# Kernel tuning notes

Measured on AMD Instinct MI355X. Metric: run time of the kernel, lower is better.

The kernel has to match this reference:

```python
import jax, jax.numpy as jnp
import numpy as np

N = 12288
IN_C = 64
OUT_C = 64
NEG_INF = -1.0e9

def setup_inputs() -> dict:
    key = jax.random.key(0)
    k1, k2, k3, k4 = jax.random.split(key, 4)
    x = jax.random.normal(k1, (N, IN_C), dtype=jnp.float32)
    edge_index = jax.random.randint(k2, (N, N), 0, 2, dtype=jnp.int32)
    # xavier-ish scaling for params
    weight_w = jax.random.normal(k3, (IN_C, OUT_C), dtype=jnp.float32) * (1.0 / np.sqrt(IN_C))
    weight_a = jax.random.normal(k4, (2 * OUT_C, 1), dtype=jnp.float32) * (1.0 / np.sqrt(OUT_C))
    bias = jnp.zeros((OUT_C,), dtype=jnp.float32)
    return {"x": x, "edge_index": edge_index, "weight_w": weight_w,
            "weight_a": weight_a, "bias": bias}

def reference(x, edge_index, weight_w, weight_a, bias):
    wh = x @ weight_w                              # [N, out]
    a_src = weight_a[:OUT_C, 0]                    # [out]
    a_dst = weight_a[OUT_C:, 0]                    # [out]
    # rank-1 additive score: e[i,j] = <wh_i, a_src> + <wh_j, a_dst>
    e = (wh @ a_src)[:, None] + (wh @ a_dst)[None, :]   # [N, N]
    e = jax.nn.leaky_relu(e, negative_slope=0.01)        # torch LeakyReLU default
    scores = jnp.where(edge_index > 0, e, NEG_INF)
    attention = jax.nn.softmax(scores, axis=1)           # row-wise
    out = attention @ wh                                  # [N, out]
    return out + bias
```

## Files before the change

kernel.cpp:

```cpp
#include <hip/hip_runtime.h>
#include <hip/hip_bf16.h>
#include <cstddef>
#include <cstdint>

#define Nn 12288
#define MSTRIDE 260
#define DSTOFF (2 * 16 * MSTRIDE)
#define LOG2E 1.44269504088896340736f

typedef __bf16 bf16x8 __attribute__((ext_vector_type(8)));
typedef float  f32x4  __attribute__((ext_vector_type(4)));
typedef int    i32x4  __attribute__((ext_vector_type(4)));

__device__ __forceinline__ void gload_lds16(const void* g, void* l) {
    __builtin_amdgcn_global_load_lds(
        (const __attribute__((address_space(1))) void*)g,
        (__attribute__((address_space(3))) void*)l, 16, 0, 0 );
}
__device__ __forceinline__ void gload_lds4(const void* g, void* l) {
    __builtin_amdgcn_global_load_lds(
        (const __attribute__((address_space(1))) void*)g,
        (__attribute__((address_space(3))) void*)l, 4, 0, 0);
}

__global__ __launch_bounds__(256) void prep_kernel(
    const float* __restrict__ x, const float* __restrict__ W,
    const float* __restrict__ wa, __bf16* __restrict__ whB,
    float* __restrict__ src, float* __restrict__ dst)
{
    __shared__ float  Wl[64 * 64];
    __shared__ float  Xl[64 * 64];
    __shared__ __bf16 whl[64 * 72];
    int t = threadIdx.x;
    int R0 = blockIdx.x * 64;
    for (int i = t; i < 4096; i += 256) {
        Wl[i] = W[i];
        Xl[i] = x[(size_t)R0 * 64 + i];
    }
    __syncthreads();
    int c   = t & 63;
    int r16 = (t >> 6) * 16;
    float vals[16];
    #pragma unroll
    for (int k = 0; k < 16; ++k) vals[k] = 0.f;
    #pragma unroll 16
    for (int kk = 0; kk < 64; ++kk) {
        float wv = Wl[kk * 64 + c];
        #pragma unroll
        for (int k = 0; k < 16; ++k)
            vals[k] = fmaf(Xl[(r16 + k) * 64 + kk], wv, vals[k]);
    }
    #pragma unroll
    for (int k = 0; k < 16; ++k) whl[c * 72 + r16 + k] = (__bf16)vals[k];
    __syncthreads();
    if (t < 64) {
        float s = 0.f, d = 0.f;
        #pragma unroll 16
        for (int cc = 0; cc < 64; ++cc) {
            float v = (float)whl[cc * 72 + t];
            s = fmaf(v, wa[cc], s);
            d = fmaf(v, wa[64 + cc], d);
        }
        src[R0 + t] = s * LOG2E;
        dst[R0 + t] = d * LOG2E;
    }
    #pragma unroll
    for (int gg = 0; gg < 2; ++gg) {
        int gidx   = t * 2 + gg;
        int jc_loc = gidx >> 8;
        int q      = (gidx >> 6) & 3;
        int lane   = gidx & 63;
        int crow   = (lane & 15) + 16 * q;
        int jrow   = jc_loc * 32 + (lane >> 4) * 8;
        bf16x8 v = *(const bf16x8*)&whl[crow * 72 + jrow];
        int jc = blockIdx.x * 2 + jc_loc;
        *(bf16x8*)&whB[((size_t)(jc * 4 + q) * 64 + lane) * 8] = v;
    }
}

__global__ __launch_bounds__(256) void attn_kernel(
    const int* __restrict__ mask, const __bf16* __restrict__ whB,
    const float* __restrict__ src, const float* __restrict__ dstv,
    const float* __restrict__ bias, float* __restrict__ out)
{
    __shared__ int lm[DSTOFF + 2 * 256];

    int t    = threadIdx.x;
    int lane = t & 63;
    int wid  = t >> 6;
    int g    = blockIdx.x;
    int row  = lane & 15;
    int kg   = lane >> 4;
    int jl   = kg * 8;

    float srow = src[g * 16 + row];
    asm volatile("" :: "v"(srow));

    bf16x8 vones;
    #pragma unroll
    for (int e = 0; e < 8; ++e) vones[e] = (__bf16)1.0f;

    i32x4 bset[2][8];
    f32x4 acc0 = {0.f, 0.f, 0.f, 0.f}, acc1 = acc0, acc2 = acc0, acc3 = acc0;
    f32x4 accZ = acc0;

#define STAGE(B, TT)                                                          \
    do {                                                                      \
        _Pragma("unroll")                                                     \
        for (int rr = 0; rr < 4; ++rr) {                                      \
            int rs = wid * 4 + rr;                                            \
            gload_lds16(mask + (size_t)(g * 16 + rs) * Nn + (TT) * 256 +      \
                            lane * 4,                                         \
                        &lm[(B) * 4160 + rs * MSTRIDE]);                      \
        }                                                                     \
        gload_lds4(dstv + (TT) * 256 + wid * 64 + lane,                       \
                   &lm[DSTOFF + (B) * 256 + wid * 64]);                       \
    } while (0)

#define BLOAD(P, TT)                                                          \
    do {                                                                      \
        const char* _b0 = (const char*)whB +                                  \
                          ((size_t)((TT) * 8 + wid * 2)) * 4096 +             \
                          (size_t)lane * 16;                                  \
        const char* _b1 = _b0 + 4096;                                         \
        asm volatile("global_load_dwordx4 %0, %1, off"                        \
                     : "=v"(bset[P][0]) : "v"(_b0));                          \
        asm volatile("global_load_dwordx4 %0, %1, off offset:1024"            \
                     : "=v"(bset[P][1]) : "v"(_b0));                          \
        asm volatile("global_load_dwordx4 %0, %1, off offset:2048"            \
                     : "=v"(bset[P][2]) : "v"(_b0));                          \
        asm volatile("global_load_dwordx4 %0, %1, off offset:3072"            \
                     : "=v"(bset[P][3]) : "v"(_b0));                          \
        asm volatile("global_load_dwordx4 %0, %1, off"                        \
                     : "=v"(bset[P][4]) : "v"(_b1));                          \
        asm volatile("global_load_dwordx4 %0, %1, off offset:1024"            \
                     : "=v"(bset[P][5]) : "v"(_b1));                          \
        asm volatile("global_load_dwordx4 %0, %1, off offset:2048"            \
                     : "=v"(bset[P][6]) : "v"(_b1));                          \
        asm volatile("global_load_dwordx4 %0, %1, off offset:3072"            \
                     : "=v"(bset[P][7]) : "v"(_b1));                          \
    } while (0)

#define COMPUTE(B, P)                                                         \
    do {                                                                      \
        const int*   mb = &lm[(B) * 4160 + row * MSTRIDE + wid * 64];         \
        const float* db = (const float*)&lm[DSTOFF + (B) * 256 + wid * 64];   \
        _Pragma("unroll")                                                     \
        for (int cc = 0; cc < 2; ++cc) {                                      \
            i32x4 m0 = *(const i32x4*)(mb + cc * 32 + jl);                    \
            i32x4 m1 = *(const i32x4*)(mb + cc * 32 + jl + 4);                \
            f32x4 d0 = *(const f32x4*)(db + cc * 32 + jl);                    \
            f32x4 d1 = *(const f32x4*)(db + cc * 32 + jl + 4);                \
            bf16x8 pa;                                                        \
            _Pragma("unroll")                                                 \
            for (int e = 0; e < 4; ++e) {                                     \
                float f0 = srow + d0[e];                                      \
                f0 = fmaxf(f0, 0.01f * f0);                                   \
                float w0 = __builtin_amdgcn_exp2f(f0);                        \
                w0 = (m0[e] > 0) ? w0 : 0.f;                                  \
                pa[e] = (__bf16)w0;                                           \
                float f1 = srow + d1[e];                                      \
                f1 = fmaxf(f1, 0.01f * f1);                                   \
                float w1 = __builtin_amdgcn_exp2f(f1);                        \
                w1 = (m1[e] > 0) ? w1 : 0.f;                                  \
                pa[4 + e] = (__bf16)w1;                                       \
            }                                                                 \
            acc0 = __builtin_amdgcn_mfma_f32_16x16x32_bf16(                   \
                pa, __builtin_bit_cast(bf16x8, bset[P][cc * 4 + 0]), acc0, 0, 0, 0); \
            acc1 = __builtin_amdgcn_mfma_f32_16x16x32_bf16(                   \
                pa, __builtin_bit_cast(bf16x8, bset[P][cc * 4 + 1]), acc1, 0, 0, 0); \
            acc2 = __builtin_amdgcn_mfma_f32_16x16x32_bf16(                   \
                pa, __builtin_bit_cast(bf16x8, bset[P][cc * 4 + 2]), acc2, 0, 0, 0); \
            acc3 = __builtin_amdgcn_mfma_f32_16x16x32_bf16(                   \
                pa, __builtin_bit_cast(bf16x8, bset[P][cc * 4 + 3]), acc3, 0, 0, 0); \
            accZ = __builtin_amdgcn_mfma_f32_16x16x32_bf16(                   \
                pa, vones, accZ, 0, 0, 0);                                    \
        }                                                                     \
    } while (0)

#define BODY_FULL(P)                                                          \
    do {                                                                      \
        STAGE((P) ^ 1, tt + 1);                                               \
        BLOAD((P) ^ 1, tt + 1);                                               \
        asm volatile("s_waitcnt vmcnt(13)" ::: "memory");                     \
        __builtin_amdgcn_sched_barrier(0);                                    \
        __builtin_amdgcn_s_barrier();                                         \
        __builtin_amdgcn_sched_barrier(0);                                    \
        COMPUTE(P, P);                                                        \
        __builtin_amdgcn_s_barrier();                                         \
        ++tt;                                                                 \
    } while (0)

    int tt = 0;
    STAGE(0, 0);
    BLOAD(0, 0);

    for (int it = 0; it < 23; ++it) {
        BODY_FULL(0);
        BODY_FULL(1);
    }
    BODY_FULL(0);
    asm volatile("s_waitcnt vmcnt(0)" ::: "memory");
    __builtin_amdgcn_sched_barrier(0);
    __builtin_amdgcn_s_barrier();
    __builtin_amdgcn_sched_barrier(0);
    COMPUTE(1, 1);

#undef BODY_FULL
#undef COMPUTE
#undef BLOAD
#undef STAGE

    __syncthreads();
    float* red  = (float*)lm;
    float* redz = red + 4096;
    #pragma unroll
    for (int r = 0; r < 4; ++r) {
        int orow = kg * 4 + r;
        red[wid * 1024 + orow * 64 + row]      = acc0[r];
        red[wid * 1024 + orow * 64 + row + 16] = acc1[r];
        red[wid * 1024 + orow * 64 + row + 32] = acc2[r];
        red[wid * 1024 + orow * 64 + row + 48] = acc3[r];
    }
    if (row == 0) {
        #pragma unroll
        for (int r = 0; r < 4; ++r) redz[wid * 16 + kg * 4 + r] = accZ[r];
    }
    __syncthreads();
    #pragma unroll
    for (int k = 0; k < 4; ++k) {
        int idx = k * 256 + t;
        int i   = idx >> 6;
        float sv = red[idx] + red[1024 + idx] + red[2048 + idx] + red[3072 + idx];
        float z  = redz[i] + redz[16 + i] + redz[32 + i] + redz[48 + i];
        z = (z != 0.f) ? z : 1.f;
        out[(size_t)g * 1024 + idx] = sv / z + bias[idx & 63];
    }
}

extern "C" void kernel_launch(void* const* d_in, const int* in_sizes, int n_in,
                              void* d_out, int out_size, void* d_ws, size_t ws_size,
                              hipStream_t stream) {
    const float* x    = (const float*)d_in[0];
    const int*   mask = (const int*)d_in[1];
    const float* W    = (const float*)d_in[2];
    const float* wa   = (const float*)d_in[3];
    const float* bias = (const float*)d_in[4];
    float* out = (float*)d_out;

    char* ws = (char*)d_ws;
    const size_t whB_bytes = (size_t)Nn * 64 * 2;
    const size_t vec_bytes = (size_t)Nn * 4;
    __bf16* whB = (__bf16*)ws;
    float*  src = (float*)(ws + whB_bytes);
    float*  dst = (float*)(ws + whB_bytes + vec_bytes);

    prep_kernel<<<Nn / 64, 256, 0, stream>>>(x, W, wa, whB, src, dst);
    attn_kernel<<<Nn / 16, 256, 0, stream>>>(mask, whB, src, dst, bias, out);
}
```

Before: 147.7 us.

## Split attention over column segments with a finalize reduction kernel

Splits the key dimension into two segments, so the grid doubles to 1536 blocks and each block handles half the columns. Partial numerators and normalizers go to workspace, and a new finalize kernel sums them, divides, and adds bias. It also marks the mask loads as nontemporal. The aim is more parallelism and shorter per-block tails on the mask stream. The cost is an extra kernel launch and extra partial-sum memory traffic.

```diff
diff --git a/kernel.cpp b/kernel.cpp
--- a/kernel.cpp
+++ b/kernel.cpp
@@ -12,10 +12,10 @@
 typedef float  f32x4  __attribute__((ext_vector_type(4)));
 typedef int    i32x4  __attribute__((ext_vector_type(4)));
 
-__device__ __forceinline__ void gload_lds16(const void* g, void* l) {
+__device__ __forceinline__ void gload_lds16_nt(const void* g, void* l) {
     __builtin_amdgcn_global_load_lds(
         (const __attribute__((address_space(1))) void*)g,
-        (__attribute__((address_space(3))) void*)l, 16, 0, 0 );
+        (__attribute__((address_space(3))) void*)l, 16, 0, 2 );
 }
 __device__ __forceinline__ void gload_lds4(const void* g, void* l) {
     __builtin_amdgcn_global_load_lds(
@@ -78,17 +78,21 @@
     }
 }
 
+template <int NSEG>
 __global__ __launch_bounds__(256) void attn_kernel(
     const int* __restrict__ mask, const __bf16* __restrict__ whB,
     const float* __restrict__ src, const float* __restrict__ dstv,
-    const float* __restrict__ bias, float* __restrict__ out)
+    float* __restrict__ pnum, float* __restrict__ pz)
 {
+    constexpr int SEGJ = Nn / NSEG;
+    constexpr int NT   = SEGJ / 256;
     __shared__ int lm[DSTOFF + 2 * 256];
 
     int t    = threadIdx.x;
     int lane = t & 63;
     int wid  = t >> 6;
-    int g    = blockIdx.x;
+    int seg  = blockIdx.x / (Nn / 16);
+    int g    = blockIdx.x % (Nn / 16);
     int row  = lane & 15;
     int kg   = lane >> 4;
     int jl   = kg * 8;
@@ -109,18 +113,19 @@
         _Pragma("unroll")                                                     \
         for (int rr = 0; rr < 4; ++rr) {                                      \
             int rs = wid * 4 + rr;                                            \
-            gload_lds16(mask + (size_t)(g * 16 + rs) * Nn + (TT) * 256 +      \
-                            lane * 4,                                         \
-                        &lm[(B) * 4160 + rs * MSTRIDE]);                      \
+            gload_lds16_nt(mask + (size_t)(g * 16 + rs) * Nn + seg * SEGJ +   \
+                               (TT) * 256 + lane * 4,                         \
+                           &lm[(B) * 4160 + rs * MSTRIDE]);                   \
         }                                                                     \
-        gload_lds4(dstv + (TT) * 256 + wid * 64 + lane,                       \
+        gload_lds4(dstv + seg * SEGJ + (TT) * 256 + wid * 64 + lane,          \
                    &lm[DSTOFF + (B) * 256 + wid * 64]);                       \
     } while (0)
 
 #define BLOAD(P, TT)                                                          \
     do {                                                                      \
         const char* _b0 = (const char*)whB +                                  \
-                          ((size_t)((TT) * 8 + wid * 2)) * 4096 +             \
+                          ((size_t)(seg * (SEGJ / 32) + (TT) * 8 + wid * 2))  \
+                              * 4096 +                                        \
                           (size_t)lane * 16;                                  \
         const char* _b1 = _b0 + 4096;                                         \
         asm volatile("global_load_dwordx4 %0, %1, off"                        \
@@ -195,7 +200,7 @@
     STAGE(0, 0);
     BLOAD(0, 0);
 
-    for (int it = 0; it < 23; ++it) {
+    for (int it = 0; it < NT / 2 - 1; ++it) {
         BODY_FULL(0);
         BODY_FULL(1);
     }
@@ -227,15 +232,32 @@
         for (int r = 0; r < 4; ++r) redz[wid * 16 + kg * 4 + r] = accZ[r];
     }
     __syncthreads();
+    size_t pb = (size_t)blockIdx.x * 1024;
     #pragma unroll
     for (int k = 0; k < 4; ++k) {
         int idx = k * 256 + t;
-        int i   = idx >> 6;
-        float sv = red[idx] + red[1024 + idx] + red[2048 + idx] + red[3072 + idx];
-        float z  = redz[i] + redz[16 + i] + redz[32 + i] + redz[48 + i];
-        z = (z != 0.f) ? z : 1.f;
-        out[(size_t)g * 1024 + idx] = sv / z + bias[idx & 63];
-    }
+        pnum[pb + idx] = red[idx] + red[1024 + idx] + red[2048 + idx] + red[3072 + idx];
+    }
+    if (t < 16)
+        pz[(size_t)blockIdx.x * 16 + t] =
+            redz[t] + redz[16 + t] + redz[32 + t] + redz[48 + t];
+}
+
+__global__ __launch_bounds__(256) void finalize_kernel(
+    const float* __restrict__ pnum, const float* __restrict__ pz,
+    const float* __restrict__ bias, float* __restrict__ out, int nseg)
+{
+    int idx = blockIdx.x * 256 + threadIdx.x;
+    int i = idx >> 6, c = idx & 63;
+    int g = i >> 4, rl = i & 15;
+    float num = 0.f, z = 0.f;
+    for (int s = 0; s < nseg; ++s) {
+        size_t b = (size_t)s * (Nn / 16) + g;
+        num += pnum[b * 1024 + rl * 64 + c];
+        z   += pz[b * 16 + rl];
+    }
+    z = (z != 0.f) ? z : 1.f;
+    out[idx] = num / z + bias[c];
 }
 
 extern "C" void kernel_launch(void* const* d_in, const int* in_sizes, int n_in,
@@ -254,7 +276,23 @@
     __bf16* whB = (__bf16*)ws;
     float*  src = (float*)(ws + whB_bytes);
     float*  dst = (float*)(ws + whB_bytes + vec_bytes);
+    size_t fixed   = whB_bytes + 2 * vec_bytes;
+    size_t per_seg = (size_t)(Nn / 16) * 1024 * 4 + (size_t)(Nn / 16) * 16 * 4;
+
+    int nseg = 2;
+    if (fixed + (size_t)nseg * per_seg > ws_size) nseg = 1;
+
+    float* pnum = (float*)(ws + fixed);
+    float* pz   = (float*)(ws + fixed + (size_t)nseg * (Nn / 16) * 1024 * 4);
 
     prep_kernel<<<Nn / 64, 256, 0, stream>>>(x, W, wa, whB, src, dst);
-    attn_kernel<<<Nn / 16, 256, 0, stream>>>(mask, whB, src, dst, bias, out);
-}
+
+    int blocks = (Nn / 16) * nseg;
+    if (nseg == 2) {
+        attn_kernel<2><<<blocks, 256, 0, stream>>>(mask, whB, src, dst, pnum, pz);
+    } else {
+        attn_kernel<1><<<blocks, 256, 0, stream>>>(mask, whB, src, dst, pnum, pz);
+    }
+
+    finalize_kernel<<<(Nn * 64) / 256, 256, 0, stream>>>(pnum, pz, bias, out, nseg);
+}
```

Measured after the change: 150.7 us. +2.0%, slower.

## Stage mask in 512-column chunks with nontemporal loads, decoupled from B pipeline

Applied to the files above, without the earlier changes.

Mask staging into LDS now brings in 512 columns per step (two compute tiles) instead of 256, uses a nontemporal cache hint, and runs on its own double buffer separate from the per-tile B and dst loads. Each wave now issues eight 1KB mask loads per pair of tiles, so mask traffic is issued in larger, less frequent batches with a deeper prefetch distance. The cost is doubled LDS for the mask buffers, which may lower occupancy, and more complex vmcnt accounting that has to stay correct for every tile.

```diff
diff --git a/kernel.cpp b/kernel.cpp
--- a/kernel.cpp
+++ b/kernel.cpp
@@ -4,18 +4,19 @@
 #include <cstdint>
 
 #define Nn 12288
-#define MSTRIDE 260
-#define DSTOFF (2 * 16 * MSTRIDE)
 #define LOG2E 1.44269504088896340736f
+#define MROWI 516
+#define MBUFI 8256
+#define DSTI  16512
 
 typedef __bf16 bf16x8 __attribute__((ext_vector_type(8)));
 typedef float  f32x4  __attribute__((ext_vector_type(4)));
 typedef int    i32x4  __attribute__((ext_vector_type(4)));
 
-__device__ __forceinline__ void gload_lds16(const void* g, void* l) {
+__device__ __forceinline__ void gload_lds16_nt(const void* g, void* l) {
     __builtin_amdgcn_global_load_lds(
         (const __attribute__((address_space(1))) void*)g,
-        (__attribute__((address_space(3))) void*)l, 16, 0, 0 );
+        (__attribute__((address_space(3))) void*)l, 16, 0, 2 );
 }
 __device__ __forceinline__ void gload_lds4(const void* g, void* l) {
     __builtin_amdgcn_global_load_lds(
@@ -83,7 +84,7 @@
     const float* __restrict__ src, const float* __restrict__ dstv,
     const float* __restrict__ bias, float* __restrict__ out)
 {
-    __shared__ int lm[DSTOFF + 2 * 256];
+    __shared__ int lm[DSTI + 2 * 256];
 
     int t    = threadIdx.x;
     int lane = t & 63;
@@ -100,51 +101,59 @@
     #pragma unroll
     for (int e = 0; e < 8; ++e) vones[e] = (__bf16)1.0f;
 
+    const char* mgb = (const char*)(mask + (size_t)g * 16 * Nn) + lane * 16;
+
     i32x4 bset[2][8];
     f32x4 acc0 = {0.f, 0.f, 0.f, 0.f}, acc1 = acc0, acc2 = acc0, acc3 = acc0;
     f32x4 accZ = acc0;
 
-#define STAGE(B, TT)                                                          \
+#define MSTAGE(SB, PR)                                                        \
     do {                                                                      \
         _Pragma("unroll")                                                     \
-        for (int rr = 0; rr < 4; ++rr) {                                      \
-            int rs = wid * 4 + rr;                                            \
-            gload_lds16(mask + (size_t)(g * 16 + rs) * Nn + (TT) * 256 +      \
-                            lane * 4,                                         \
-                        &lm[(B) * 4160 + rs * MSTRIDE]);                      \
+        for (int o = 0; o < 8; ++o) {                                         \
+            int k    = wid * 8 + o;                                           \
+            int rr   = k >> 1;                                                \
+            int half = k & 1;                                                 \
+            gload_lds16_nt(mgb + (size_t)rr * (Nn * 4) + (PR) * 2048 +        \
+                               half * 1024,                                   \
+                           (char*)lm + (SB) * (MBUFI * 4) + rr * (MROWI * 4) +\
+                               half * 1024);                                  \
         }                                                                     \
-        gload_lds4(dstv + (TT) * 256 + wid * 64 + lane,                       \
-                   &lm[DSTOFF + (B) * 256 + wid * 64]);                       \
-    } while (0)
-
-#define BLOAD(P, TT)                                                          \
+    } while (0)
+
+#define DSTAGE(PS, TT)                                                        \
+    gload_lds4(dstv + (TT) * 256 + wid * 64 + lane,                           \
+               (char*)lm + DSTI * 4 + (PS) * 1024 + wid * 256)
+
+#define BLOAD(PS, TT)                                                         \
     do {                                                                      \
         const char* _b0 = (const char*)whB +                                  \
                           ((size_t)((TT) * 8 + wid * 2)) * 4096 +             \
                           (size_t)lane * 16;                                  \
         const char* _b1 = _b0 + 4096;                                         \
         asm volatile("global_load_dwordx4 %0, %1, off"                        \
-                     : "=v"(bset[P][0]) : "v"(_b0));                          \
+                     : "=v"(bset[PS][0]) : "v"(_b0));                         \
         asm volatile("global_load_dwordx4 %0, %1, off offset:1024"            \
-                     : "=v"(bset[P][1]) : "v"(_b0));                          \
+                     : "=v"(bset[PS][1]) : "v"(_b0));                         \
         asm volatile("global_load_dwordx4 %0, %1, off offset:2048"            \
-                     : "=v"(bset[P][2]) : "v"(_b0));                          \
+                     : "=v"(bset[PS][2]) : "v"(_b0));                         \
         asm volatile("global_load_dwordx4 %0, %1, off offset:3072"            \
-                     : "=v"(bset[P][3]) : "v"(_b0));                          \
+                     : "=v"(bset[PS][3]) : "v"(_b0));                         \
         asm volatile("global_load_dwordx4 %0, %1, off"                        \
-                     : "=v"(bset[P][4]) : "v"(_b1));                          \
+                     : "=v"(bset[PS][4]) : "v"(_b1));                         \
         asm volatile("global_load_dwordx4 %0, %1, off offset:1024"            \
-                     : "=v"(bset[P][5]) : "v"(_b1));                          \
+                     : "=v"(bset[PS][5]) : "v"(_b1));                         \
         asm volatile("global_load_dwordx4 %0, %1, off offset:2048"            \
-                     : "=v"(bset[P][6]) : "v"(_b1));                          \
+                     : "=v"(bset[PS][6]) : "v"(_b1));                         \
         asm volatile("global_load_dwordx4 %0, %1, off offset:3072"            \
-                     : "=v"(bset[P][7]) : "v"(_b1));                          \
-    } while (0)
-
-#define COMPUTE(B, P)                                                         \
-    do {                                                                      \
-        const int*   mb = &lm[(B) * 4160 + row * MSTRIDE + wid * 64];         \
-        const float* db = (const float*)&lm[DSTOFF + (B) * 256 + wid * 64];   \
+                     : "=v"(bset[PS][7]) : "v"(_b1));                         \
+    } while (0)
+
+#define COMPUTE(MB, H, PS)                                                    \
+    do {                                                                      \
+        const int*   mb = &lm[(MB) * MBUFI + row * MROWI + (H) * 256 +        \
+                              wid * 64];                                      \
+        const float* db = (const float*)&lm[DSTI + (PS) * 256 + wid * 64];    \
         _Pragma("unroll")                                                     \
         for (int cc = 0; cc < 2; ++cc) {                                      \
             i32x4 m0 = *(const i32x4*)(mb + cc * 32 + jl);                    \
@@ -166,50 +175,70 @@
                 pa[4 + e] = (__bf16)w1;                                       \
             }                                                                 \
             acc0 = __builtin_amdgcn_mfma_f32_16x16x32_bf16(                   \
-                pa, __builtin_bit_cast(bf16x8, bset[P][cc * 4 + 0]), acc0, 0, 0, 0); \
+                pa, __builtin_bit_cast(bf16x8, bset[PS][cc * 4 + 0]), acc0, 0, 0, 0); \
             acc1 = __builtin_amdgcn_mfma_f32_16x16x32_bf16(                   \
-                pa, __builtin_bit_cast(bf16x8, bset[P][cc * 4 + 1]), acc1, 0, 0, 0); \
+                pa, __builtin_bit_cast(bf16x8, bset[PS][cc * 4 + 1]), acc1, 0, 0, 0); \
             acc2 = __builtin_amdgcn_mfma_f32_16x16x32_bf16(                   \
-                pa, __builtin_bit_cast(bf16x8, bset[P][cc * 4 + 2]), acc2, 0, 0, 0); \
+                pa, __builtin_bit_cast(bf16x8, bset[PS][cc * 4 + 2]), acc2, 0, 0, 0); \
             acc3 = __builtin_amdgcn_mfma_f32_16x16x32_bf16(                   \
-                pa, __builtin_bit_cast(bf16x8, bset[P][cc * 4 + 3]), acc3, 0, 0, 0); \
+                pa, __builtin_bit_cast(bf16x8, bset[PS][cc * 4 + 3]), acc3, 0, 0, 0); \
             accZ = __builtin_amdgcn_mfma_f32_16x16x32_bf16(                   \
                 pa, vones, accZ, 0, 0, 0);                                    \
         }                                                                     \
     } while (0)
 
-#define BODY_FULL(P)                                                          \
-    do {                                                                      \
-        STAGE((P) ^ 1, tt + 1);                                               \
-        BLOAD((P) ^ 1, tt + 1);                                               \
-        asm volatile("s_waitcnt vmcnt(13)" ::: "memory");                     \
+#define WAITBAR(N)                                                            \
+    do {                                                                      \
+        asm volatile("s_waitcnt vmcnt(" #N ")" ::: "memory");                 \
         __builtin_amdgcn_sched_barrier(0);                                    \
         __builtin_amdgcn_s_barrier();                                         \
         __builtin_amdgcn_sched_barrier(0);                                    \
-        COMPUTE(P, P);                                                        \
+    } while (0)
+
+#define PAIR_BODY(MB, SB)                                                     \
+    do {                                                                      \
+        BLOAD(1, tt + 1);                                                     \
+        DSTAGE(1, tt + 1);                                                    \
+        MSTAGE(SB, pr + 1);                                                   \
+        WAITBAR(17);                                                          \
+        COMPUTE(MB, 0, 0);                                                    \
         __builtin_amdgcn_s_barrier();                                         \
         ++tt;                                                                 \
-    } while (0)
-
-    int tt = 0;
-    STAGE(0, 0);
+        BLOAD(0, tt + 1);                                                     \
+        DSTAGE(0, tt + 1);                                                    \
+        WAITBAR(17);                                                          \
+        COMPUTE(MB, 1, 1);                                                    \
+        __builtin_amdgcn_s_barrier();                                         \
+        ++tt;                                                                 \
+        ++pr;                                                                 \
+    } while (0)
+
+    int tt = 0, pr = 0;
+    MSTAGE(0, 0);
+    DSTAGE(0, 0);
     BLOAD(0, 0);
-
-    for (int it = 0; it < 23; ++it) {
-        BODY_FULL(0);
-        BODY_FULL(1);
-    }
-    BODY_FULL(0);
-    asm volatile("s_waitcnt vmcnt(0)" ::: "memory");
     __builtin_amdgcn_sched_barrier(0);
+
+    for (int it = 0; it < 11; ++it) {
+        PAIR_BODY(0, 1);
+        PAIR_BODY(1, 0);
+    }
+    PAIR_BODY(0, 1);
+
+    BLOAD(1, tt + 1);
+    DSTAGE(1, tt + 1);
+    WAITBAR(9);
+    COMPUTE(1, 0, 0);
     __builtin_amdgcn_s_barrier();
-    __builtin_amdgcn_sched_barrier(0);
-    COMPUTE(1, 1);
-
-#undef BODY_FULL
+    WAITBAR(0);
+    COMPUTE(1, 1, 1);
+
+#undef PAIR_BODY
+#undef WAITBAR
 #undef COMPUTE
 #undef BLOAD
-#undef STAGE
+#undef DSTAGE
+#undef MSTAGE
 
     __syncthreads();
     float* red  = (float*)lm;
```

Measured after the change: 140.0 us. -5.2%, faster.
